# Kernel tuning notes

Hardware: AMD Instinct MI355X
Metric: run time of the kernel (lower is better)

## Reference

```python
import jax, jax.numpy as jnp
import numpy as np

B, N, FEAT = 64, 1024, 3
HID, STATE, LAYERS, NTYPES = 64, 32, 2, 10


def setup_inputs() -> dict:
    key = jax.random.key(0)
    ks = jax.random.split(key, 16)
    s = 0.1
    return {
        "task_features": jax.random.normal(ks[0], (B, N, FEAT), jnp.float32),
        "task_types": jax.random.randint(ks[1], (B, N), 0, NTYPES, jnp.int32),
        "prev_state": jnp.zeros((B, STATE), jnp.float32),
        "enc_w1": jax.random.normal(ks[2], (HID, FEAT), jnp.float32) * s,
        "enc_b1": jnp.zeros((HID,), jnp.float32),
        "enc_w2": jax.random.normal(ks[3], (HID, HID), jnp.float32) * s,
        "enc_b2": jnp.zeros((HID,), jnp.float32),
        "contention": jax.random.normal(ks[4], (NTYPES, NTYPES), jnp.float32) * 0.1,
        "gnn_w": jax.random.normal(ks[5], (LAYERS, HID, HID), jnp.float32) * s,
        "gnn_b": jnp.zeros((LAYERS, HID), jnp.float32),
        "gru_w_ih": jax.random.normal(ks[6], (3 * STATE, HID), jnp.float32) * s,
        "gru_w_hh": jax.random.normal(ks[7], (3 * STATE, STATE), jnp.float32) * s,
        "gru_b_ih": jnp.zeros((3 * STATE,), jnp.float32),
        "gru_b_hh": jnp.zeros((3 * STATE,), jnp.float32),
        "head_w1": jax.random.normal(ks[8], (HID, HID + STATE), jnp.float32) * s,
        "head_b1": jnp.zeros((HID,), jnp.float32),
        "head_w2": jax.random.normal(ks[9], (1, HID), jnp.float32) * s,
        "head_b2": jnp.zeros((1,), jnp.float32),
    }


def _forward(task_features, task_types, prev_state, enc_w1, enc_b1, enc_w2, enc_b2,
             contention, gnn_w, gnn_b, gru_w_ih, gru_w_hh, gru_b_ih, gru_b_hh,
             head_w1, head_b1, head_w2, head_b2):
    # task encoder: Linear -> ReLU -> Linear
    emb = jax.nn.relu(task_features @ enc_w1.T + enc_b1) @ enc_w2.T + enc_b2  # (B,N,H)
    # interaction graph: type-pair gather + cosine similarity
    base = contention[task_types[:, :, None], task_types[:, None, :]]  # (B,N,N)
    nrm = emb / jnp.maximum(jnp.linalg.norm(emb, axis=-1, keepdims=True), 1e-12)
    sim = jnp.einsum("bnd,bmd->bnm", nrm, nrm)
    adjacency = jax.nn.sigmoid(base) * sim  # (B,N,N)
    # GNN layers: aggregate + linear + relu
    h = emb
    for l in range(LAYERS):
        agg = jnp.einsum("bnm,bmd->bnd", adjacency, h)
        h = jax.nn.relu((h + agg) @ gnn_w[l].T + gnn_b[l])
    ctx = h.mean(axis=1)  # (B,H)
    # GRUCell (torch semantics)
    gi = ctx @ gru_w_ih.T + gru_b_ih
    gh = prev_state @ gru_w_hh.T + gru_b_hh
    i_r, i_z, i_n = jnp.split(gi, 3, axis=-1)
    h_r, h_z, h_n = jnp.split(gh, 3, axis=-1)
    r = jax.nn.sigmoid(i_r + h_r)
    z = jax.nn.sigmoid(i_z + h_z)
    n = jnp.tanh(i_n + r * h_n)
    new_state = (1.0 - z) * n + z * prev_state  # (B,S)
    # latency head on [h, state]
    st = jnp.broadcast_to(new_state[:, None, :], (h.shape[0], h.shape[1], new_state.shape[-1]))
    combined = jnp.concatenate([h, st], axis=-1)
    lat = jax.nn.relu(combined @ head_w1.T + head_b1) @ head_w2.T + head_b2
    return lat[..., 0], new_state


def reference(task_features, task_types, prev_state, enc_w1, enc_b1, enc_w2, enc_b2,
              contention, gnn_w, gnn_b, gru_w_ih, gru_w_hh, gru_b_ih, gru_b_hh,
              head_w1, head_b1, head_w2, head_b2):
    return _forward(task_features, task_types, prev_state, enc_w1, enc_b1, enc_w2, enc_b2,
                    contention, gnn_w, gnn_b, gru_w_ih, gru_w_hh, gru_b_ih, gru_b_hh,
                    head_w1, head_b1, head_w2, head_b2)
```

## Files before the change

### kernel.cpp

```cpp
#include <hip/hip_runtime.h>
#include <math.h>

#define BB 64
#define NN 1024
#define HID 64
#define STATE 32
#define NTYPES 10

typedef _Float16 f16;
typedef f16 f16x8 __attribute__((ext_vector_type(8)));
typedef f16 f16x4 __attribute__((ext_vector_type(4)));
typedef float f32x4 __attribute__((ext_vector_type(4)));

#define MFMA16(a, b, c) __builtin_amdgcn_mfma_f32_16x16x32_f16(a, b, c, 0, 0, 0)

__device__ __forceinline__ float sigm(float x) { return 1.f / (1.f + expf(-x)); }

__device__ __forceinline__ f16x8 cvt8(float4 a, float4 b) {
    f16x8 r;
    r[0] = (f16)a.x; r[1] = (f16)a.y; r[2] = (f16)a.z; r[3] = (f16)a.w;
    r[4] = (f16)b.x; r[5] = (f16)b.y; r[6] = (f16)b.z; r[7] = (f16)b.w;
    return r;
}
__device__ __forceinline__ unsigned packh2(f16 a, f16 b) {
    union { f16 h[2]; unsigned u; } p;
    p.h[0] = a; p.h[1] = b;
    return p.u;
}

__global__ __launch_bounds__(256) void k_misc(
    const float* __restrict__ w2, const float* __restrict__ gw,
    const float* __restrict__ hw1, f16* __restrict__ out,
    int* __restrict__ cnt, float* __restrict__ ctx)
{
    int p = blockIdx.x * 256 + threadIdx.x;
    if (p < 18432) {
        const float* W; int K, pl;
        if (p < 12288) { int seg = p >> 12; pl = p & 4095; W = (seg == 0) ? w2 : gw + (seg - 1) * 4096; K = 64; }
        else { W = hw1; K = 96; pl = p - 12288; }
        int j = pl & 7, lane = (pl >> 3) & 63, nt = (pl >> 9) & 3, ch = pl >> 11;
        int k = ch * 32 + ((lane >> 4) << 3) + j;
        int o = nt * 16 + (lane & 15);
        out[p] = (f16)W[o * K + k];
        return;
    }
    int q = p - 18432;
    if (q < BB * NTYPES) { cnt[q] = 0; return; }
    q -= BB * NTYPES;
    if (q < BB * HID) ctx[q] = 0.f;
}

__global__ __launch_bounds__(256) void k_encoder(
    const float* __restrict__ feat,
    const float* __restrict__ w1, const float* __restrict__ b1,
    const f16* __restrict__ w2f, const float* __restrict__ b2,
    const int* __restrict__ types, int* __restrict__ idx, int* __restrict__ cnt,
    f16* __restrict__ nrm, float* __restrict__ sclv)
{
    __shared__ f16 w2s[4096];
    __shared__ f16 tmp[4][16 * 72];
    __shared__ float fbuf[4][48];
    int tid = threadIdx.x, wave = tid >> 6, lane = tid & 63;
    int l15 = lane & 15, quad = lane >> 4;
    if (tid < 64) {
        int row = blockIdx.x * 64 + tid;
        int b = row >> 10;
        int t = types[row];
        int pos = atomicAdd(&cnt[b * NTYPES + t], 1);
        idx[(b * NTYPES + t) * NN + pos] = row & (NN - 1);
    }
    { const uint4* s = (const uint4*)w2f; uint4* d = (uint4*)w2s;
      for (int i = tid; i < 512; i += 256) d[i] = s[i]; }
    float w10 = w1[lane * 3], w11 = w1[lane * 3 + 1], w12 = w1[lane * 3 + 2], b1l = b1[lane];
    int tb = blockIdx.x * 64 + wave * 16;
    if (lane < 48) fbuf[wave][lane] = feat[tb * 3 + lane];
    __syncthreads();
    f16* tw = &tmp[wave][0];
#pragma unroll
    for (int r = 0; r < 16; ++r) {
        float x0 = fbuf[wave][r * 3], x1 = fbuf[wave][r * 3 + 1], x2 = fbuf[wave][r * 3 + 2];
        float hv = fmaxf(fmaf(w10, x0, fmaf(w11, x1, fmaf(w12, x2, b1l))), 0.f);
        tw[r * 72 + lane] = (f16)hv;
    }
    __builtin_amdgcn_sched_barrier(0);
    f16x8 a0 = *(const f16x8*)&tw[l15 * 72 + quad * 8];
    f16x8 a1 = *(const f16x8*)&tw[l15 * 72 + 32 + quad * 8];
    const f16x8* bf = (const f16x8*)w2s;
    f32x4 acc[4];
#pragma unroll
    for (int nt = 0; nt < 4; ++nt) {
        f32x4 c = {0.f, 0.f, 0.f, 0.f};
        c = MFMA16(a0, bf[(0 * 4 + nt) * 64 + lane], c);
        c = MFMA16(a1, bf[(1 * 4 + nt) * 64 + lane], c);
        acc[nt] = c;
    }
    float b2c[4];
#pragma unroll
    for (int nt = 0; nt < 4; ++nt) b2c[nt] = b2[nt * 16 + l15];
#pragma unroll
    for (int i = 0; i < 4; ++i) {
        float v[4]; float ss = 0.f;
#pragma unroll
        for (int nt = 0; nt < 4; ++nt) { v[nt] = acc[nt][i] + b2c[nt]; ss = fmaf(v[nt], v[nt], ss); }
        ss += __shfl_xor(ss, 1, 64); ss += __shfl_xor(ss, 2, 64);
        ss += __shfl_xor(ss, 4, 64); ss += __shfl_xor(ss, 8, 64);
        float nm = fmaxf(sqrtf(ss), 1e-12f);
        float rinv = 1.f / nm;
        int grow = tb + quad * 4 + i;
#pragma unroll
        for (int nt = 0; nt < 4; ++nt)
            nrm[(size_t)grow * 64 + nt * 16 + l15] = (f16)(v[nt] * rinv);
        if (l15 == 0) sclv[grow] = nm;
    }
}

#define TSTR2 72
__global__ __launch_bounds__(256) void k_buildM(
    const int* __restrict__ idx, const int* __restrict__ cnt,
    const f16* __restrict__ nrm, const f16* __restrict__ h,
    const float* __restrict__ scale, f16* __restrict__ M)
{
    __shared__ f16 nT[64 * TSTR2];
    __shared__ f16 hT[64 * TSTR2];
    int bj = blockIdx.x;
    int b = bj / NTYPES;
    int c = cnt[bj];
    const int* lst = idx + (size_t)bj * NN;
    int tid = threadIdx.x, wave = tid >> 6, lane = tid & 63;
    int l15 = lane & 15, quad = lane >> 4;
    int r = tid & 15;
    int q4 = tid >> 4;
    const f16* nb = nrm + (size_t)b * NN * 64;
    const f16* hb = h + (size_t)b * NN * 64;
    const float* sb = scale ? scale + (size_t)b * NN : nullptr;
    f32x4 acc[4] = {{0.f,0.f,0.f,0.f},{0.f,0.f,0.f,0.f},{0.f,0.f,0.f,0.f},{0.f,0.f,0.f,0.f}};
    for (int k0 = 0; k0 < c; k0 += 64) {
        __syncthreads();
        f16x4 a[4], g[4];
#pragma unroll
        for (int u = 0; u < 4; ++u) { a[u] = (f16x4){0,0,0,0}; g[u] = (f16x4){0,0,0,0}; }
#pragma unroll
        for (int u = 0; u < 4; ++u) {
            int mi = k0 + 4 * r + u;
            if (mi < c) {
                int m = lst[mi];
                a[u] = *(const f16x4*)&nb[(size_t)m * 64 + 4 * q4];
                if (sb) { f16 sm = (f16)sb[m]; f16x4 sv = {sm, sm, sm, sm}; g[u] = a[u] * sv; }
                else g[u] = *(const f16x4*)&hb[(size_t)m * 64 + 4 * q4];
            }
        }
#pragma unroll
        for (int i = 0; i < 4; ++i) {
            *(unsigned*)&nT[(4 * q4 + i) * TSTR2 + 4 * r]     = packh2(a[0][i], a[1][i]);
            *(unsigned*)&nT[(4 * q4 + i) * TSTR2 + 4 * r + 2] = packh2(a[2][i], a[3][i]);
            *(unsigned*)&hT[(4 * q4 + i) * TSTR2 + 4 * r]     = packh2(g[0][i], g[1][i]);
            *(unsigned*)&hT[(4 * q4 + i) * TSTR2 + 4 * r + 2] = packh2(g[2][i], g[3][i]);
        }
        __syncthreads();
        f16x8 af0 = *(const f16x8*)&nT[(wave * 16 + l15) * TSTR2 + quad * 8];
        f16x8 af1 = *(const f16x8*)&nT[(wave * 16 + l15) * TSTR2 + 32 + quad * 8];
#pragma unroll
        for (int nt = 0; nt < 4; ++nt) {
            f16x8 bf0 = *(const f16x8*)&hT[(nt * 16 + l15) * TSTR2 + quad * 8];
            f16x8 bf1 = *(const f16x8*)&hT[(nt * 16 + l15) * TSTR2 + 32 + quad * 8];
            acc[nt] = MFMA16(af0, bf0, acc[nt]);
            acc[nt] = MFMA16(af1, bf1, acc[nt]);
        }
    }
    f16* Mo = M + (size_t)bj * 4096;
#pragma unroll
    for (int nt = 0; nt < 4; ++nt)
#pragma unroll
        for (int i = 0; i < 4; ++i)
            Mo[(wave * 16 + quad * 4 + i) * 64 + nt * 16 + l15] = (f16)acc[nt][i];
}

__global__ __launch_bounds__(256) void k_gnn0_fused(
    const int* __restrict__ idx, const int* __restrict__ cnt,
    const float* __restrict__ cont, const f16* __restrict__ M,
    const f16* __restrict__ nrm, const float* __restrict__ scale,
    const f16* __restrict__ gwf, const float* __restrict__ gb,
    f16* __restrict__ hout, f16* __restrict__ Mout)
{
    __shared__ f16 ds_[4096];
    __shared__ f16 gs[4096];
    __shared__ __align__(16) f16 nT[64 * TSTR2];
    __shared__ __align__(16) f16 hT[64 * TSTR2];
    int i0 = blockIdx.x;
    int xcd = i0 & 7, k = i0 >> 3;
    int b = xcd + 8 * (k / NTYPES);
    int t = k % NTYPES;
    int bt = b * NTYPES + t;
    int c = cnt[bt];
    int tid = threadIdx.x, wave = tid >> 6, lane = tid & 63;
    int l15 = lane & 15, quad = lane >> 4;
    { const uint4* s2 = (const uint4*)gwf; uint4* d2 = (uint4*)gs;
      for (int i = tid; i < 512; i += 256) d2[i] = s2[i]; }
    float sg[NTYPES];
#pragma unroll
    for (int j = 0; j < NTYPES; ++j) sg[j] = sigm(cont[t * NTYPES + j]);
    float ca[16];
#pragma unroll
    for (int i = 0; i < 16; ++i) ca[i] = 0.f;
    const f16* Mb = M + (size_t)b * NTYPES * 4096;
#pragma unroll
    for (int j = 0; j < NTYPES; ++j) {
        const f16* Mr = Mb + j * 4096 + (wave * 16 + l15) * 64;
        f16x8 m0 = *(const f16x8*)&Mr[quad * 8];
        f16x8 m1 = *(const f16x8*)&Mr[32 + quad * 8];
        float sv = sg[j];
#pragma unroll
        for (int e = 0; e < 8; ++e) {
            ca[e]     = fmaf(sv, (float)m0[e], ca[e]);
            ca[8 + e] = fmaf(sv, (float)m1[e], ca[8 + e]);
        }
    }
    f16x8 ca0, ca1;
#pragma unroll
    for (int i = 0; i < 8; ++i) { ca0[i] = (f16)ca[i]; ca1[i] = (f16)ca[8 + i]; }
    __syncthreads();
    const f16x8* gbf = (const f16x8*)gs;
#pragma unroll
    for (int nt = 0; nt < 4; ++nt) {
        f32x4 dd = {0.f, 0.f, 0.f, 0.f};
        dd = MFMA16(ca0, gbf[(0 * 4 + nt) * 64 + lane], dd);
        dd = MFMA16(ca1, gbf[(1 * 4 + nt) * 64 + lane], dd);
#pragma unroll
        for (int i = 0; i < 4; ++i) {
            int d = wave * 16 + quad * 4 + i;
            int pos = (((d >> 5) * 4 + nt) * 64 + ((d >> 3) & 3) * 16 + l15) * 8 + (d & 7);
            ds_[pos] = (f16)dd[i];
        }
    }
    __syncthreads();
    float gbl[4];
#pragma unroll
    for (int nt = 0; nt < 4; ++nt) gbl[nt] = gb[nt * 16 + l15];
    const int* lst = idx + (size_t)bt * NN;
    const f16* nb = nrm + (size_t)b * NN * 64;
    const float* sb = scale + (size_t)b * NN;
    f16* hob = hout + (size_t)b * NN * 64;
    const f16x8* dbf = (const f16x8*)ds_;
    f32x4 macc[4];
#pragma unroll
    for (int nt = 0; nt < 4; ++nt) macc[nt] = (f32x4){0.f, 0.f, 0.f, 0.f};
    int nchunk = (c + 63) >> 6;
    for (int ch = 0; ch < nchunk; ++ch) {
        int tb = ch * 64 + wave * 16;
        int rA = tb + l15;
        bool okA = rA < c;
        int mA = lst[okA ? rA : (c - 1)];
        const f16* na = nb + (size_t)mA * 64;
        f16x8 a0 = *(const f16x8*)&na[quad * 8];
        f16x8 a1 = *(const f16x8*)&na[32 + quad * 8];
        f32x4 acc1[4], acc2[4];
#pragma unroll
        for (int nt = 0; nt < 4; ++nt) {
            f32x4 c1 = {0.f, 0.f, 0.f, 0.f}, c2 = {0.f, 0.f, 0.f, 0.f};
            c1 = MFMA16(a0, dbf[(0 * 4 + nt) * 64 + lane], c1);
            c1 = MFMA16(a1, dbf[(1 * 4 + nt) * 64 + lane], c1);
            c2 = MFMA16(a0, gbf[(0 * 4 + nt) * 64 + lane], c2);
            c2 = MFMA16(a1, gbf[(1 * 4 + nt) * 64 + lane], c2);
            acc1[nt] = c1; acc2[nt] = c2;
        }
        f16x4 hv[4];
#pragma unroll
        for (int nt = 0; nt < 4; ++nt) hv[nt] = (f16x4){0, 0, 0, 0};
#pragma unroll
        for (int i = 0; i < 4; ++i) {
            int rr = tb + quad * 4 + i;
            if (rr < c) {
                int m = lst[rr];
                float sm = sb[m];
#pragma unroll
                for (int nt = 0; nt < 4; ++nt) {
                    float v = fmaxf(fmaf(sm, acc2[nt][i], acc1[nt][i]) + gbl[nt], 0.f);
                    f16 vh = (f16)v;
                    hob[(size_t)m * 64 + nt * 16 + l15] = vh;
                    hv[nt][i] = vh;
                }
            }
        }
        f16x8 z8 = {0, 0, 0, 0, 0, 0, 0, 0};
        f16x8 s0 = okA ? a0 : z8;
        f16x8 s1 = okA ? a1 : z8;
#pragma unroll
        for (int j = 0; j < 8; ++j) {
            nT[(quad * 8 + j) * TSTR2 + wave * 16 + l15]      = s0[j];
            nT[(32 + quad * 8 + j) * TSTR2 + wave * 16 + l15] = s1[j];
        }
#pragma unroll
        for (int nt = 0; nt < 4; ++nt)
            *(f16x4*)&hT[(nt * 16 + l15) * TSTR2 + wave * 16 + quad * 4] = hv[nt];
        __syncthreads();
        f16x8 af0 = *(const f16x8*)&nT[(wave * 16 + l15) * TSTR2 + quad * 8];
        f16x8 af1 = *(const f16x8*)&nT[(wave * 16 + l15) * TSTR2 + 32 + quad * 8];
#pragma unroll
        for (int nt = 0; nt < 4; ++nt) {
            f16x8 bf0 = *(const f16x8*)&hT[(nt * 16 + l15) * TSTR2 + quad * 8];
            f16x8 bf1 = *(const f16x8*)&hT[(nt * 16 + l15) * TSTR2 + 32 + quad * 8];
            macc[nt] = MFMA16(af0, bf0, macc[nt]);
            macc[nt] = MFMA16(af1, bf1, macc[nt]);
        }
        __syncthreads();
    }
    f16* Mo = Mout + (size_t)bt * 4096;
#pragma unroll
    for (int nt = 0; nt < 4; ++nt)
#pragma unroll
        for (int i = 0; i < 4; ++i)
            Mo[(wave * 16 + quad * 4 + i) * 64 + nt * 16 + l15] = (f16)macc[nt][i];
}

__global__ __launch_bounds__(256) void k_gnn_layer(
    const int* __restrict__ idx, const int* __restrict__ cnt,
    const float* __restrict__ cont, const f16* __restrict__ M,
    const f16* __restrict__ nrm, const f16* __restrict__ h,
    const float* __restrict__ scale,
    const f16* __restrict__ gwf, const float* __restrict__ gb,
    f16* __restrict__ hout, float* __restrict__ ctx)
{
    __shared__ f16 ds_[4096];
    __shared__ f16 gs[4096];
    int i0 = blockIdx.x;
    int xcd = i0 & 7, k = i0 >> 3;
    int b = xcd + 8 * (k / NTYPES);
    int t = k % NTYPES;
    int bt = b * NTYPES + t;
    int c = cnt[bt];
    if (c == 0) return;
    int tid = threadIdx.x, wave = tid >> 6, lane = tid & 63;
    int l15 = lane & 15, quad = lane >> 4;
    { const uint4* s2 = (const uint4*)gwf; uint4* d2 = (uint4*)gs;
      for (int i = tid; i < 512; i += 256) d2[i] = s2[i]; }
    float sg[NTYPES];
#pragma unroll
    for (int j = 0; j < NTYPES; ++j) sg[j] = sigm(cont[t * NTYPES + j]);
    float ca[16];
#pragma unroll
    for (int i = 0; i < 16; ++i) ca[i] = 0.f;
    const f16* Mb = M + (size_t)b * NTYPES * 4096;
#pragma unroll
    for (int j = 0; j < NTYPES; ++j) {
        const f16* Mr = Mb + j * 4096 + (wave * 16 + l15) * 64;
        f16x8 m0 = *(const f16x8*)&Mr[quad * 8];
        f16x8 m1 = *(const f16x8*)&Mr[32 + quad * 8];
        float sv = sg[j];
#pragma unroll
        for (int e = 0; e < 8; ++e) {
            ca[e]     = fmaf(sv, (float)m0[e], ca[e]);
            ca[8 + e] = fmaf(sv, (float)m1[e], ca[8 + e]);
        }
    }
    f16x8 ca0, ca1;
#pragma unroll
    for (int i = 0; i < 8; ++i) { ca0[i] = (f16)ca[i]; ca1[i] = (f16)ca[8 + i]; }
    __syncthreads();
    const f16x8* gbf = (const f16x8*)gs;
#pragma unroll
    for (int nt = 0; nt < 4; ++nt) {
        f32x4 dd = {0.f, 0.f, 0.f, 0.f};
        dd = MFMA16(ca0, gbf[(0 * 4 + nt) * 64 + lane], dd);
        dd = MFMA16(ca1, gbf[(1 * 4 + nt) * 64 + lane], dd);
#pragma unroll
        for (int i = 0; i < 4; ++i) {
            int d = wave * 16 + quad * 4 + i;
            int pos = (((d >> 5) * 4 + nt) * 64 + ((d >> 3) & 3) * 16 + l15) * 8 + (d & 7);
            ds_[pos] = (f16)dd[i];
        }
    }
    __syncthreads();
    float gbl[4];
#pragma unroll
    for (int nt = 0; nt < 4; ++nt) gbl[nt] = gb[nt * 16 + l15];
    const int* lst = idx + (size_t)bt * NN;
    const f16* nb = nrm + (size_t)b * NN * 64;
    const f16* hb = h + (size_t)b * NN * 64;
    f16* hob = hout + (size_t)b * NN * 64;
    const f16x8* dbf = (const f16x8*)ds_;
    float cacc[4] = {0.f, 0.f, 0.f, 0.f};
    for (int g = wave; g * 16 < c; g += 4) {
        int tb = g * 16;
        int rA = tb + l15; if (rA >= c) rA = c - 1;
        int mA = lst[rA];
        const f16* na = nb + (size_t)mA * 64;
        f16x8 a0 = *(const f16x8*)&na[quad * 8];
        f16x8 a1 = *(const f16x8*)&na[32 + quad * 8];
        const f16* ha = hb + (size_t)mA * 64;
        f16x8 h0 = *(const f16x8*)&ha[quad * 8];
        f16x8 h1 = *(const f16x8*)&ha[32 + quad * 8];
        f32x4 acc[4];
#pragma unroll
        for (int nt = 0; nt < 4; ++nt) {
            f32x4 cc = {0.f, 0.f, 0.f, 0.f};
            cc = MFMA16(a0, dbf[(0 * 4 + nt) * 64 + lane], cc);
            cc = MFMA16(a1, dbf[(1 * 4 + nt) * 64 + lane], cc);
            cc = MFMA16(h0, gbf[(0 * 4 + nt) * 64 + lane], cc);
            cc = MFMA16(h1, gbf[(1 * 4 + nt) * 64 + lane], cc);
            acc[nt] = cc;
        }
#pragma unroll
        for (int i = 0; i < 4; ++i) {
            int rr = tb + quad * 4 + i;
            if (rr < c) {
                int m = lst[rr];
#pragma unroll
                for (int nt = 0; nt < 4; ++nt) {
                    float v = fmaxf(acc[nt][i] + gbl[nt], 0.f);
                    hob[(size_t)m * 64 + nt * 16 + l15] = (f16)v;
                    cacc[nt] += v;
                }
            }
        }
    }
    if (ctx) {
#pragma unroll
        for (int nt = 0; nt < 4; ++nt) {
            float sv = cacc[nt];
            sv += __shfl_xor(sv, 16, 64);
            sv += __shfl_xor(sv, 32, 64);
            if (quad == 0) atomicAdd(&ctx[b * HID + nt * 16 + l15], sv);
        }
    }
}

__global__ __launch_bounds__(256) void k_head(
    const f16* __restrict__ h2, const float* __restrict__ ctx_sum,
    const float* __restrict__ prev,
    const float* __restrict__ w_ih, const float* __restrict__ w_hh,
    const float* __restrict__ b_ih, const float* __restrict__ b_hh,
    const f16* __restrict__ hwf, const float* __restrict__ b1,
    const float* __restrict__ w2, const float* __restrict__ b2,
    float* __restrict__ lat, float* __restrict__ state_out)
{
    __shared__ f16 ws_[6144];
    __shared__ __align__(16) float st[STATE];
    __shared__ float cs[HID], ps[STATE], gis[96], ghs[96];
    int tid = threadIdx.x, wave = tid >> 6, lane = tid & 63;
    int l15 = lane & 15, quad = lane >> 4;
    int b = blockIdx.x >> 4;
    { const uint4* s = (const uint4*)hwf; uint4* d = (uint4*)ws_;
      for (int i = tid; i < 768; i += 256) d[i] = s[i]; }
    if (tid < HID) cs[tid] = ctx_sum[b * HID + tid] * (1.f / NN);
    if (tid >= HID && tid < HID + STATE) ps[tid - HID] = prev[b * STATE + tid - HID];
    __syncthreads();
    if (tid < 96) {
        float gi = b_ih[tid];
#pragma unroll 8
        for (int k = 0; k < HID; ++k) gi = fmaf(w_ih[tid * HID + k], cs[k], gi);
        float gh = b_hh[tid];
#pragma unroll
        for (int k = 0; k < STATE; ++k) gh = fmaf(w_hh[tid * STATE + k], ps[k], gh);
        gis[tid] = gi; ghs[tid] = gh;
    }
    __syncthreads();
    if (tid < STATE) {
        float r = sigm(gis[tid] + ghs[tid]);
        float z = sigm(gis[32 + tid] + ghs[32 + tid]);
        float nn = tanhf(gis[64 + tid] + r * ghs[64 + tid]);
        float v = (1.f - z) * nn + z * ps[tid];
        st[tid] = v;
        if ((blockIdx.x & 15) == 0) state_out[b * STATE + tid] = v;
    }
    __syncthreads();
    float b1c[4], w2c[4];
#pragma unroll
    for (int nt = 0; nt < 4; ++nt) { b1c[nt] = b1[nt * 16 + l15]; w2c[nt] = w2[nt * 16 + l15]; }
    float b2v = b2[0];
    int tb = blockIdx.x * 64 + wave * 16;
    int grow = tb + l15;
    const f16* ha = h2 + (size_t)grow * 64;
    f16x8 a0 = *(const f16x8*)&ha[quad * 8];
    f16x8 a1 = *(const f16x8*)&ha[32 + quad * 8];
    const float4* sp = (const float4*)st;
    f16x8 a2 = cvt8(sp[quad * 2], sp[quad * 2 + 1]);
    const f16x8* bf = (const f16x8*)ws_;
    f32x4 acc[4];
#pragma unroll
    for (int nt = 0; nt < 4; ++nt) {
        f32x4 cc = {0.f, 0.f, 0.f, 0.f};
        cc = MFMA16(a0, bf[(0 * 4 + nt) * 64 + lane], cc);
        cc = MFMA16(a1, bf[(1 * 4 + nt) * 64 + lane], cc);
        cc = MFMA16(a2, bf[(2 * 4 + nt) * 64 + lane], cc);
        acc[nt] = cc;
    }
#pragma unroll
    for (int i = 0; i < 4; ++i) {
        float s = 0.f;
#pragma unroll
        for (int nt = 0; nt < 4; ++nt) s = fmaf(fmaxf(acc[nt][i] + b1c[nt], 0.f), w2c[nt], s);
        s += __shfl_xor(s, 1, 64); s += __shfl_xor(s, 2, 64);
        s += __shfl_xor(s, 4, 64); s += __shfl_xor(s, 8, 64);
        if (l15 == 0) lat[tb + quad * 4 + i] = s + b2v;
    }
}

extern "C" void kernel_launch(void* const* d_in, const int* in_sizes, int n_in,
                              void* d_out, int out_size, void* d_ws, size_t ws_size,
                              hipStream_t stream) {
    const float* feat   = (const float*)d_in[0];
    const int*   types  = (const int*)d_in[1];
    const float* prev   = (const float*)d_in[2];
    const float* enc_w1 = (const float*)d_in[3];
    const float* enc_b1 = (const float*)d_in[4];
    const float* enc_w2 = (const float*)d_in[5];
    const float* enc_b2 = (const float*)d_in[6];
    const float* cont   = (const float*)d_in[7];
    const float* gnn_w  = (const float*)d_in[8];
    const float* gnn_b  = (const float*)d_in[9];
    const float* w_ih   = (const float*)d_in[10];
    const float* w_hh   = (const float*)d_in[11];
    const float* b_ih   = (const float*)d_in[12];
    const float* b_hh   = (const float*)d_in[13];
    const float* hw1    = (const float*)d_in[14];
    const float* hb1    = (const float*)d_in[15];
    const float* hw2    = (const float*)d_in[16];
    const float* hb2    = (const float*)d_in[17];
    float* out = (float*)d_out;

    float* ws  = (float*)d_ws;
    f16*   nrm = (f16*)ws;
    f16*   h1  = (f16*)(ws + 2097152);
    f16*   h2  = (f16*)(ws + 4194304);
    float* scl = ws + 6291456;
    int*   idx = (int*)(ws + 6356992);
    int*   cnt = idx + BB * NTYPES * NN;
    f16*   M0  = (f16*)(ws + 7012992);
    f16*   M1  = (f16*)(ws + 8323712);
    f16*   wfrag = (f16*)(ws + 9634432);
    float* ctx   = ws + 9643648;
    f16*   w2f  = wfrag;
    f16*   gw0f = wfrag + 4096;
    f16*   gw1f = wfrag + 8192;
    f16*   hwf  = wfrag + 12288;

    k_misc<<<91, 256, 0, stream>>>(enc_w2, gnn_w, hw1, wfrag, cnt, ctx);
    k_encoder<<<BB * NN / 64, 256, 0, stream>>>(feat, enc_w1, enc_b1, w2f, enc_b2,
                                                types, idx, cnt, nrm, scl);
    k_buildM<<<BB * NTYPES, 256, 0, stream>>>(idx, cnt, nrm, nrm, scl, M0);
    k_gnn0_fused<<<BB * NTYPES, 256, 0, stream>>>(idx, cnt, cont, M0, nrm, scl,
                                                  gw0f, gnn_b, h1, M1);
    k_gnn_layer<<<BB * NTYPES, 256, 0, stream>>>(idx, cnt, cont, M1, nrm, h1, nullptr,
                                                 gw1f, gnn_b + HID, h2, ctx);
    k_head<<<BB * NN / 64, 256, 0, stream>>>(h2, ctx, prev, w_ih, w_hh, b_ih, b_hh,
                                             hwf, hb1, hw2, hb2, out, out + BB * NN);
}
```

Baseline: 169.1 us.

## Store activations packed per batch-type bucket and drop weight-swizzle kernel

The encoder now scatters normalized embeddings and scales straight into contiguous per-(batch, type) buckets of fixed capacity 256. Later GNN kernels can then read rows directly instead of gathering them through an index list. The separate weight-swizzle and zeroing kernel is removed: each kernel swizzles its own weights into shared memory, ctx is zeroed inside the encoder, and counts are cleared with a memset. The head kernel runs per bucket and scatters latencies back through the index list. The fixed capacity assumes no type appears more than 256 times in a batch, and every block now repeats the weight conversion work.

```diff
diff --git a/kernel.cpp b/kernel.cpp
--- a/kernel.cpp
+++ b/kernel.cpp
@@ -6,6 +6,8 @@
 #define HID 64
 #define STATE 32
 #define NTYPES 10
+#define CAP 256
+#define CAPE (CAP * 64)
 
 typedef _Float16 f16;
 typedef f16 f16x8 __attribute__((ext_vector_type(8)));
@@ -28,49 +30,40 @@
     return p.u;
 }
 
-__global__ __launch_bounds__(256) void k_misc(
-    const float* __restrict__ w2, const float* __restrict__ gw,
-    const float* __restrict__ hw1, f16* __restrict__ out,
-    int* __restrict__ cnt, float* __restrict__ ctx)
-{
-    int p = blockIdx.x * 256 + threadIdx.x;
-    if (p < 18432) {
-        const float* W; int K, pl;
-        if (p < 12288) { int seg = p >> 12; pl = p & 4095; W = (seg == 0) ? w2 : gw + (seg - 1) * 4096; K = 64; }
-        else { W = hw1; K = 96; pl = p - 12288; }
-        int j = pl & 7, lane = (pl >> 3) & 63, nt = (pl >> 9) & 3, ch = pl >> 11;
-        int k = ch * 32 + ((lane >> 4) << 3) + j;
-        int o = nt * 16 + (lane & 15);
-        out[p] = (f16)W[o * K + k];
-        return;
-    }
-    int q = p - 18432;
-    if (q < BB * NTYPES) { cnt[q] = 0; return; }
-    q -= BB * NTYPES;
-    if (q < BB * HID) ctx[q] = 0.f;
+__device__ __forceinline__ void swz_load(const float* __restrict__ W, int K, int n,
+                                         f16* dst, int tid) {
+    for (int p = tid; p < n; p += 256) {
+        int j = p & 7, ln = (p >> 3) & 63, nt = (p >> 9) & 3, ch = p >> 11;
+        int k = ch * 32 + ((ln >> 4) << 3) + j;
+        int o = nt * 16 + (ln & 15);
+        dst[p] = (f16)W[o * K + k];
+    }
 }
 
 __global__ __launch_bounds__(256) void k_encoder(
     const float* __restrict__ feat,
     const float* __restrict__ w1, const float* __restrict__ b1,
-    const f16* __restrict__ w2f, const float* __restrict__ b2,
+    const float* __restrict__ w2, const float* __restrict__ b2,
     const int* __restrict__ types, int* __restrict__ idx, int* __restrict__ cnt,
-    f16* __restrict__ nrm, float* __restrict__ sclv)
+    f16* __restrict__ nrmp, float* __restrict__ sclp, float* __restrict__ ctx)
 {
     __shared__ f16 w2s[4096];
     __shared__ f16 tmp[4][16 * 72];
     __shared__ float fbuf[4][48];
+    __shared__ int pkbuf[64];
     int tid = threadIdx.x, wave = tid >> 6, lane = tid & 63;
     int l15 = lane & 15, quad = lane >> 4;
     if (tid < 64) {
         int row = blockIdx.x * 64 + tid;
         int b = row >> 10;
         int t = types[row];
-        int pos = atomicAdd(&cnt[b * NTYPES + t], 1);
-        idx[(b * NTYPES + t) * NN + pos] = row & (NN - 1);
-    }
-    { const uint4* s = (const uint4*)w2f; uint4* d = (uint4*)w2s;
-      for (int i = tid; i < 512; i += 256) d[i] = s[i]; }
+        int bt = b * NTYPES + t;
+        int pos = atomicAdd(&cnt[bt], 1);
+        idx[bt * CAP + pos] = row & (NN - 1);
+        pkbuf[tid] = bt * CAP + pos;
+    }
+    if (blockIdx.x < 16) ctx[blockIdx.x * 256 + tid] = 0.f;
+    swz_load(w2, 64, 4096, w2s, tid);
     float w10 = w1[lane * 3], w11 = w1[lane * 3 + 1], w12 = w1[lane * 3 + 2], b1l = b1[lane];
     int tb = blockIdx.x * 64 + wave * 16;
     if (lane < 48) fbuf[wave][lane] = feat[tb * 3 + lane];
@@ -106,33 +99,32 @@
         ss += __shfl_xor(ss, 4, 64); ss += __shfl_xor(ss, 8, 64);
         float nm = fmaxf(sqrtf(ss), 1e-12f);
         float rinv = 1.f / nm;
-        int grow = tb + quad * 4 + i;
+        int pk = pkbuf[wave * 16 + quad * 4 + i];
 #pragma unroll
         for (int nt = 0; nt < 4; ++nt)
-            nrm[(size_t)grow * 64 + nt * 16 + l15] = (f16)(v[nt] * rinv);
-        if (l15 == 0) sclv[grow] = nm;
+            nrmp[(size_t)pk * 64 + nt * 16 + l15] = (f16)(v[nt] * rinv);
+        if (l15 == 0) sclp[pk] = nm;
     }
 }
 
 #define TSTR2 72
-__global__ __launch_bounds__(256) void k_buildM(
-    const int* __restrict__ idx, const int* __restrict__ cnt,
-    const f16* __restrict__ nrm, const f16* __restrict__ h,
-    const float* __restrict__ scale, f16* __restrict__ M)
+__global__ __launch_bounds__(256) void k_buildM0(
+    const int* __restrict__ cnt, const f16* __restrict__ nrmp,
+    const float* __restrict__ sclp, f16* __restrict__ M0)
 {
     __shared__ f16 nT[64 * TSTR2];
     __shared__ f16 hT[64 * TSTR2];
-    int bj = blockIdx.x;
-    int b = bj / NTYPES;
-    int c = cnt[bj];
-    const int* lst = idx + (size_t)bj * NN;
+    int i0 = blockIdx.x;
+    int xcd = i0 & 7, kk = i0 >> 3;
+    int b = xcd + 8 * (kk / NTYPES);
+    int t = kk % NTYPES;
+    int bt = b * NTYPES + t;
+    int c = cnt[bt];
     int tid = threadIdx.x, wave = tid >> 6, lane = tid & 63;
     int l15 = lane & 15, quad = lane >> 4;
-    int r = tid & 15;
-    int q4 = tid >> 4;
-    const f16* nb = nrm + (size_t)b * NN * 64;
-    const f16* hb = h + (size_t)b * NN * 64;
-    const float* sb = scale ? scale + (size_t)b * NN : nullptr;
+    int r = tid & 15, q4 = tid >> 4;
+    const f16* nb = nrmp + (size_t)bt * CAPE;
+    const float* sb = sclp + (size_t)bt * CAP;
     f32x4 acc[4] = {{0.f,0.f,0.f,0.f},{0.f,0.f,0.f,0.f},{0.f,0.f,0.f,0.f},{0.f,0.f,0.f,0.f}};
     for (int k0 = 0; k0 < c; k0 += 64) {
         __syncthreads();
@@ -143,10 +135,9 @@
         for (int u = 0; u < 4; ++u) {
             int mi = k0 + 4 * r + u;
             if (mi < c) {
-                int m = lst[mi];
-                a[u] = *(const f16x4*)&nb[(size_t)m * 64 + 4 * q4];
-                if (sb) { f16 sm = (f16)sb[m]; f16x4 sv = {sm, sm, sm, sm}; g[u] = a[u] * sv; }
-                else g[u] = *(const f16x4*)&hb[(size_t)m * 64 + 4 * q4];
+                a[u] = *(const f16x4*)&nb[(size_t)mi * 64 + 4 * q4];
+                f16 sm = (f16)sb[mi]; f16x4 sv = {sm, sm, sm, sm};
+                g[u] = a[u] * sv;
             }
         }
 #pragma unroll
@@ -167,7 +158,7 @@
             acc[nt] = MFMA16(af1, bf1, acc[nt]);
         }
     }
-    f16* Mo = M + (size_t)bj * 4096;
+    f16* Mo = M0 + (size_t)bt * 4096;
 #pragma unroll
     for (int nt = 0; nt < 4; ++nt)
 #pragma unroll
@@ -176,26 +167,25 @@
 }
 
 __global__ __launch_bounds__(256) void k_gnn0_fused(
-    const int* __restrict__ idx, const int* __restrict__ cnt,
-    const float* __restrict__ cont, const f16* __restrict__ M,
-    const f16* __restrict__ nrm, const float* __restrict__ scale,
-    const f16* __restrict__ gwf, const float* __restrict__ gb,
-    f16* __restrict__ hout, f16* __restrict__ Mout)
+    const int* __restrict__ cnt, const float* __restrict__ cont,
+    const f16* __restrict__ M, const f16* __restrict__ nrmp,
+    const float* __restrict__ sclp,
+    const float* __restrict__ gw, const float* __restrict__ gb,
+    f16* __restrict__ h1p, f16* __restrict__ Mout)
 {
     __shared__ f16 ds_[4096];
     __shared__ f16 gs[4096];
     __shared__ __align__(16) f16 nT[64 * TSTR2];
     __shared__ __align__(16) f16 hT[64 * TSTR2];
     int i0 = blockIdx.x;
-    int xcd = i0 & 7, k = i0 >> 3;
-    int b = xcd + 8 * (k / NTYPES);
-    int t = k % NTYPES;
+    int xcd = i0 & 7, kk = i0 >> 3;
+    int b = xcd + 8 * (kk / NTYPES);
+    int t = kk % NTYPES;
     int bt = b * NTYPES + t;
     int c = cnt[bt];
     int tid = threadIdx.x, wave = tid >> 6, lane = tid & 63;
     int l15 = lane & 15, quad = lane >> 4;
-    { const uint4* s2 = (const uint4*)gwf; uint4* d2 = (uint4*)gs;
-      for (int i = tid; i < 512; i += 256) d2[i] = s2[i]; }
+    swz_load(gw, 64, 4096, gs, tid);
     float sg[NTYPES];
 #pragma unroll
     for (int j = 0; j < NTYPES; ++j) sg[j] = sigm(cont[t * NTYPES + j]);
@@ -236,10 +226,9 @@
     float gbl[4];
 #pragma unroll
     for (int nt = 0; nt < 4; ++nt) gbl[nt] = gb[nt * 16 + l15];
-    const int* lst = idx + (size_t)bt * NN;
-    const f16* nb = nrm + (size_t)b * NN * 64;
-    const float* sb = scale + (size_t)b * NN;
-    f16* hob = hout + (size_t)b * NN * 64;
+    const f16* nb = nrmp + (size_t)bt * CAPE;
+    const float* sb = sclp + (size_t)bt * CAP;
+    f16* hob = h1p + (size_t)bt * CAPE;
     const f16x8* dbf = (const f16x8*)ds_;
     f32x4 macc[4];
 #pragma unroll
@@ -249,8 +238,8 @@
         int tb = ch * 64 + wave * 16;
         int rA = tb + l15;
         bool okA = rA < c;
-        int mA = lst[okA ? rA : (c - 1)];
-        const f16* na = nb + (size_t)mA * 64;
+        int rAc = okA ? rA : (c - 1);
+        const f16* na = nb + (size_t)rAc * 64;
         f16x8 a0 = *(const f16x8*)&na[quad * 8];
         f16x8 a1 = *(const f16x8*)&na[32 + quad * 8];
         f32x4 acc1[4], acc2[4];
@@ -270,13 +259,12 @@
         for (int i = 0; i < 4; ++i) {
             int rr = tb + quad * 4 + i;
             if (rr < c) {
-                int m = lst[rr];
-                float sm = sb[m];
+                float sm = sb[rr];
 #pragma unroll
                 for (int nt = 0; nt < 4; ++nt) {
                     float v = fmaxf(fmaf(sm, acc2[nt][i], acc1[nt][i]) + gbl[nt], 0.f);
                     f16 vh = (f16)v;
-                    hob[(size_t)m * 64 + nt * 16 + l15] = vh;
+                    hob[(size_t)rr * 64 + nt * 16 + l15] = vh;
                     hv[nt][i] = vh;
                 }
             }
@@ -312,27 +300,25 @@
             Mo[(wave * 16 + quad * 4 + i) * 64 + nt * 16 + l15] = (f16)macc[nt][i];
 }
 
-__global__ __launch_bounds__(256) void k_gnn_layer(
-    const int* __restrict__ idx, const int* __restrict__ cnt,
-    const float* __restrict__ cont, const f16* __restrict__ M,
-    const f16* __restrict__ nrm, const f16* __restrict__ h,
-    const float* __restrict__ scale,
-    const f16* __restrict__ gwf, const float* __restrict__ gb,
-    f16* __restrict__ hout, float* __restrict__ ctx)
+__global__ __launch_bounds__(256) void k_gnn1(
+    const int* __restrict__ cnt, const float* __restrict__ cont,
+    const f16* __restrict__ M, const f16* __restrict__ nrmp,
+    const f16* __restrict__ h1p,
+    const float* __restrict__ gw, const float* __restrict__ gb,
+    f16* __restrict__ h2p, float* __restrict__ ctx)
 {
     __shared__ f16 ds_[4096];
     __shared__ f16 gs[4096];
     int i0 = blockIdx.x;
-    int xcd = i0 & 7, k = i0 >> 3;
-    int b = xcd + 8 * (k / NTYPES);
-    int t = k % NTYPES;
+    int xcd = i0 & 7, kk = i0 >> 3;
+    int b = xcd + 8 * (kk / NTYPES);
+    int t = kk % NTYPES;
     int bt = b * NTYPES + t;
     int c = cnt[bt];
     if (c == 0) return;
     int tid = threadIdx.x, wave = tid >> 6, lane = tid & 63;
     int l15 = lane & 15, quad = lane >> 4;
-    { const uint4* s2 = (const uint4*)gwf; uint4* d2 = (uint4*)gs;
-      for (int i = tid; i < 512; i += 256) d2[i] = s2[i]; }
+    swz_load(gw, 64, 4096, gs, tid);
     float sg[NTYPES];
 #pragma unroll
     for (int j = 0; j < NTYPES; ++j) sg[j] = sigm(cont[t * NTYPES + j]);
@@ -373,20 +359,18 @@
     float gbl[4];
 #pragma unroll
     for (int nt = 0; nt < 4; ++nt) gbl[nt] = gb[nt * 16 + l15];
-    const int* lst = idx + (size_t)bt * NN;
-    const f16* nb = nrm + (size_t)b * NN * 64;
-    const f16* hb = h + (size_t)b * NN * 64;
-    f16* hob = hout + (size_t)b * NN * 64;
+    const f16* nb = nrmp + (size_t)bt * CAPE;
+    const f16* hb = h1p + (size_t)bt * CAPE;
+    f16* hob = h2p + (size_t)bt * CAPE;
     const f16x8* dbf = (const f16x8*)ds_;
     float cacc[4] = {0.f, 0.f, 0.f, 0.f};
     for (int g = wave; g * 16 < c; g += 4) {
         int tb = g * 16;
         int rA = tb + l15; if (rA >= c) rA = c - 1;
-        int mA = lst[rA];
-        const f16* na = nb + (size_t)mA * 64;
+        const f16* na = nb + (size_t)rA * 64;
         f16x8 a0 = *(const f16x8*)&na[quad * 8];
         f16x8 a1 = *(const f16x8*)&na[32 + quad * 8];
-        const f16* ha = hb + (size_t)mA * 64;
+        const f16* ha = hb + (size_t)rA * 64;
         f16x8 h0 = *(const f16x8*)&ha[quad * 8];
         f16x8 h1 = *(const f16x8*)&ha[32 + quad * 8];
         f32x4 acc[4];
@@ -403,44 +387,46 @@
         for (int i = 0; i < 4; ++i) {
             int rr = tb + quad * 4 + i;
             if (rr < c) {
-                int m = lst[rr];
 #pragma unroll
                 for (int nt = 0; nt < 4; ++nt) {
                     float v = fmaxf(acc[nt][i] + gbl[nt], 0.f);
-                    hob[(size_t)m * 64 + nt * 16 + l15] = (f16)v;
+                    hob[(size_t)rr * 64 + nt * 16 + l15] = (f16)v;
                     cacc[nt] += v;
                 }
             }
         }
     }
-    if (ctx) {
-#pragma unroll
-        for (int nt = 0; nt < 4; ++nt) {
-            float sv = cacc[nt];
-            sv += __shfl_xor(sv, 16, 64);
-            sv += __shfl_xor(sv, 32, 64);
-            if (quad == 0) atomicAdd(&ctx[b * HID + nt * 16 + l15], sv);
-        }
+#pragma unroll
+    for (int nt = 0; nt < 4; ++nt) {
+        float sv = cacc[nt];
+        sv += __shfl_xor(sv, 16, 64);
+        sv += __shfl_xor(sv, 32, 64);
+        if (quad == 0) atomicAdd(&ctx[b * HID + nt * 16 + l15], sv);
     }
 }
 
 __global__ __launch_bounds__(256) void k_head(
-    const f16* __restrict__ h2, const float* __restrict__ ctx_sum,
+    const f16* __restrict__ h2p, const int* __restrict__ idx,
+    const int* __restrict__ cnt, const float* __restrict__ ctx_sum,
     const float* __restrict__ prev,
     const float* __restrict__ w_ih, const float* __restrict__ w_hh,
     const float* __restrict__ b_ih, const float* __restrict__ b_hh,
-    const f16* __restrict__ hwf, const float* __restrict__ b1,
+    const float* __restrict__ hw1, const float* __restrict__ b1,
     const float* __restrict__ w2, const float* __restrict__ b2,
     float* __restrict__ lat, float* __restrict__ state_out)
 {
     __shared__ f16 ws_[6144];
     __shared__ __align__(16) float st[STATE];
     __shared__ float cs[HID], ps[STATE], gis[96], ghs[96];
+    int i0 = blockIdx.x;
+    int xcd = i0 & 7, kk = i0 >> 3;
+    int b = xcd + 8 * (kk / NTYPES);
+    int t = kk % NTYPES;
+    int bt = b * NTYPES + t;
+    int c = cnt[bt];
     int tid = threadIdx.x, wave = tid >> 6, lane = tid & 63;
     int l15 = lane & 15, quad = lane >> 4;
-    int b = blockIdx.x >> 4;
-    { const uint4* s = (const uint4*)hwf; uint4* d = (uint4*)ws_;
-      for (int i = tid; i < 768; i += 256) d[i] = s[i]; }
+    swz_load(hw1, 96, 6144, ws_, tid);
     if (tid < HID) cs[tid] = ctx_sum[b * HID + tid] * (1.f / NN);
     if (tid >= HID && tid < HID + STATE) ps[tid - HID] = prev[b * STATE + tid - HID];
     __syncthreads();
@@ -460,38 +446,47 @@
         float nn = tanhf(gis[64 + tid] + r * ghs[64 + tid]);
         float v = (1.f - z) * nn + z * ps[tid];
         st[tid] = v;
-        if ((blockIdx.x & 15) == 0) state_out[b * STATE + tid] = v;
-    }
-    __syncthreads();
+        if (t == 0) state_out[b * STATE + tid] = v;
+    }
+    __syncthreads();
+    if (c == 0) return;
     float b1c[4], w2c[4];
 #pragma unroll
     for (int nt = 0; nt < 4; ++nt) { b1c[nt] = b1[nt * 16 + l15]; w2c[nt] = w2[nt * 16 + l15]; }
     float b2v = b2[0];
-    int tb = blockIdx.x * 64 + wave * 16;
-    int grow = tb + l15;
-    const f16* ha = h2 + (size_t)grow * 64;
-    f16x8 a0 = *(const f16x8*)&ha[quad * 8];
-    f16x8 a1 = *(const f16x8*)&ha[32 + quad * 8];
     const float4* sp = (const float4*)st;
     f16x8 a2 = cvt8(sp[quad * 2], sp[quad * 2 + 1]);
     const f16x8* bf = (const f16x8*)ws_;
-    f32x4 acc[4];
-#pragma unroll
-    for (int nt = 0; nt < 4; ++nt) {
-        f32x4 cc = {0.f, 0.f, 0.f, 0.f};
-        cc = MFMA16(a0, bf[(0 * 4 + nt) * 64 + lane], cc);
-        cc = MFMA16(a1, bf[(1 * 4 + nt) * 64 + lane], cc);
-        cc = MFMA16(a2, bf[(2 * 4 + nt) * 64 + lane], cc);
-        acc[nt] = cc;
-    }
-#pragma unroll
-    for (int i = 0; i < 4; ++i) {
-        float s = 0.f;
-#pragma unroll
-        for (int nt = 0; nt < 4; ++nt) s = fmaf(fmaxf(acc[nt][i] + b1c[nt], 0.f), w2c[nt], s);
-        s += __shfl_xor(s, 1, 64); s += __shfl_xor(s, 2, 64);
-        s += __shfl_xor(s, 4, 64); s += __shfl_xor(s, 8, 64);
-        if (l15 == 0) lat[tb + quad * 4 + i] = s + b2v;
+    const f16* hb = h2p + (size_t)bt * CAPE;
+    const int* lst = idx + (size_t)bt * CAP;
+    for (int g = wave; g * 16 < c; g += 4) {
+        int tb = g * 16;
+        int rA = tb + l15; if (rA >= c) rA = c - 1;
+        const f16* ha = hb + (size_t)rA * 64;
+        f16x8 a0 = *(const f16x8*)&ha[quad * 8];
+        f16x8 a1 = *(const f16x8*)&ha[32 + quad * 8];
+        f32x4 acc[4];
+#pragma unroll
+        for (int nt = 0; nt < 4; ++nt) {
+            f32x4 cc = {0.f, 0.f, 0.f, 0.f};
+            cc = MFMA16(a0, bf[(0 * 4 + nt) * 64 + lane], cc);
+            cc = MFMA16(a1, bf[(1 * 4 + nt) * 64 + lane], cc);
+            cc = MFMA16(a2, bf[(2 * 4 + nt) * 64 + lane], cc);
+            acc[nt] = cc;
+        }
+#pragma unroll
+        for (int i = 0; i < 4; ++i) {
+            float s = 0.f;
+#pragma unroll
+            for (int nt = 0; nt < 4; ++nt) s = fmaf(fmaxf(acc[nt][i] + b1c[nt], 0.f), w2c[nt], s);
+            s += __shfl_xor(s, 1, 64); s += __shfl_xor(s, 2, 64);
+            s += __shfl_xor(s, 4, 64); s += __shfl_xor(s, 8, 64);
+            int rr = tb + quad * 4 + i;
+            if (l15 == 0 && rr < c) {
+                int m = lst[rr];
+                lat[b * NN + m] = s + b2v;
+            }
+        }
     }
 }
 
@@ -518,30 +513,26 @@
     const float* hb2    = (const float*)d_in[17];
     float* out = (float*)d_out;
 
-    float* ws  = (float*)d_ws;
-    f16*   nrm = (f16*)ws;
-    f16*   h1  = (f16*)(ws + 2097152);
-    f16*   h2  = (f16*)(ws + 4194304);
-    float* scl = ws + 6291456;
-    int*   idx = (int*)(ws + 6356992);
-    int*   cnt = idx + BB * NTYPES * NN;
-    f16*   M0  = (f16*)(ws + 7012992);
-    f16*   M1  = (f16*)(ws + 8323712);
-    f16*   wfrag = (f16*)(ws + 9634432);
-    float* ctx   = ws + 9643648;
-    f16*   w2f  = wfrag;
-    f16*   gw0f = wfrag + 4096;
-    f16*   gw1f = wfrag + 8192;
-    f16*   hwf  = wfrag + 12288;
-
-    k_misc<<<91, 256, 0, stream>>>(enc_w2, gnn_w, hw1, wfrag, cnt, ctx);
-    k_encoder<<<BB * NN / 64, 256, 0, stream>>>(feat, enc_w1, enc_b1, w2f, enc_b2,
-                                                types, idx, cnt, nrm, scl);
-    k_buildM<<<BB * NTYPES, 256, 0, stream>>>(idx, cnt, nrm, nrm, scl, M0);
-    k_gnn0_fused<<<BB * NTYPES, 256, 0, stream>>>(idx, cnt, cont, M0, nrm, scl,
-                                                  gw0f, gnn_b, h1, M1);
-    k_gnn_layer<<<BB * NTYPES, 256, 0, stream>>>(idx, cnt, cont, M1, nrm, h1, nullptr,
-                                                 gw1f, gnn_b + HID, h2, ctx);
-    k_head<<<BB * NN / 64, 256, 0, stream>>>(h2, ctx, prev, w_ih, w_hh, b_ih, b_hh,
-                                             hwf, hb1, hw2, hb2, out, out + BB * NN);
-}
+    float* ws   = (float*)d_ws;
+    f16*   nrmp = (f16*)ws;
+    f16*   h1p  = (f16*)(ws + 5242880);
+    f16*   h2p  = (f16*)(ws + 10485760);
+    float* sclp = ws + 15728640;
+    int*   idx  = (int*)(ws + 15892480);
+    int*   cnt  = (int*)(ws + 16056320);
+    f16*   M0   = (f16*)(ws + 16057344);
+    f16*   M1   = (f16*)(ws + 17368064);
+    float* ctx  = ws + 18678784;
+
+    hipMemsetAsync(cnt, 0, BB * NTYPES * sizeof(int), stream);
+    k_encoder<<<BB * NN / 64, 256, 0, stream>>>(feat, enc_w1, enc_b1, enc_w2, enc_b2,
+                                                types, idx, cnt, nrmp, sclp, ctx);
+    k_buildM0<<<BB * NTYPES, 256, 0, stream>>>(cnt, nrmp, sclp, M0);
+    k_gnn0_fused<<<BB * NTYPES, 256, 0, stream>>>(cnt, cont, M0, nrmp, sclp,
+                                                  gnn_w, gnn_b, h1p, M1);
+    k_gnn1<<<BB * NTYPES, 256, 0, stream>>>(cnt, cont, M1, nrmp, h1p,
+                                            gnn_w + 4096, gnn_b + HID, h2p, ctx);
+    k_head<<<BB * NTYPES, 256, 0, stream>>>(h2p, idx, cnt, ctx, prev,
+                                            w_ih, w_hh, b_ih, b_hh,
+                                            hw1, hb1, hw2, hb2, out, out + BB * NN);
+}
```

Result: no change. 165.8 us (-1.9%).
